# Performance work log

Hardware: AMD Instinct MI355X
Metric: run time of the kernel (lower is better)

Reference implementation:

```python
import jax, jax.numpy as jnp
import numpy as np

N_NODES = 50000
N_EDGES = 800000
D_IN = 128
HIDDEN = 64
N_CLASSES = 2


def gcn_conv(x, edge_index, W, b, num_nodes):
    """PyG GCNConv: linear (no bias) -> add self-loops -> sym-normalized aggregate -> + bias."""
    h = x @ W  # [N, H]
    loop = jnp.arange(num_nodes, dtype=edge_index.dtype)
    src = jnp.concatenate([edge_index[0], loop])  # [E+N]
    dst = jnp.concatenate([edge_index[1], loop])
    deg = jax.ops.segment_sum(jnp.ones_like(dst, dtype=h.dtype), dst, num_segments=num_nodes)
    dinv = jnp.where(deg > 0, jax.lax.rsqrt(deg), 0.0)
    norm = dinv[src] * dinv[dst]  # [E+N]
    msg = h[src] * norm[:, None]  # [E+N, H]  (gather + scale)
    out = jax.ops.segment_sum(msg, dst, num_segments=num_nodes)  # scatter-add
    return out + b


def setup_inputs() -> dict:
    key = jax.random.key(0)
    ks = jax.random.split(key, 6)
    x = jax.random.normal(ks[0], (N_NODES, D_IN), dtype=jnp.float32)
    edge_index = jax.random.randint(ks[1], (2, N_EDGES), 0, N_NODES, dtype=jnp.int64)
    # Glorot-ish init for weights, zero bias (PyG default)
    W1 = jax.random.normal(ks[2], (D_IN, HIDDEN), dtype=jnp.float32) * (1.0 / np.sqrt(D_IN))
    b1 = jnp.zeros((HIDDEN,), dtype=jnp.float32)
    W2 = jax.random.normal(ks[3], (HIDDEN, N_CLASSES), dtype=jnp.float32) * (1.0 / np.sqrt(HIDDEN))
    b2 = jnp.zeros((N_CLASSES,), dtype=jnp.float32)
    return {"x": x, "edge_index": edge_index, "W1": W1, "b1": b1, "W2": W2, "b2": b2}


def reference(x, edge_index, W1, b1, W2, b2):
    h = jax.nn.relu(gcn_conv(x, edge_index, W1, b1, N_NODES))
    # F.dropout(training=self.training) is identity in eval mode
    out = gcn_conv(h, edge_index, W2, b2, N_NODES)
    return out
```

## Files before the change

### kernel.cpp

```cpp
#include <hip/hip_runtime.h>

#define N_NODES 50000
#define N_EDGES 800000
#define D_IN 128
#define HIDDEN 64
#define N_CLASSES 2
#define NBUK 782
#define NBUK_P 784
#define NBLK 196
#define NBLK_P 200
#define NE4 200000
#define XPAD 136

typedef _Float16 half4v __attribute__((ext_vector_type(4)));
typedef _Float16 h8 __attribute__((ext_vector_type(8)));
typedef float f4 __attribute__((ext_vector_type(4)));


__global__ __launch_bounds__(256) void k_hist(const int4* __restrict__ dst4,
                                              int* __restrict__ bhist) {
    __shared__ int hist[NBUK];
    int t = threadIdx.x;
    for (int i = t; i < NBUK; i += 256) hist[i] = 0;
    __syncthreads();
    int base4 = blockIdx.x * 1024;
#pragma unroll
    for (int k = 0; k < 4; k++) {
        int idx = base4 + k * 256 + t;
        if (idx < NE4) {
            int4 d = dst4[idx];
            atomicAdd(&hist[d.x >> 6], 1);
            atomicAdd(&hist[d.y >> 6], 1);
            atomicAdd(&hist[d.z >> 6], 1);
            atomicAdd(&hist[d.w >> 6], 1);
        }
    }
    __syncthreads();
    for (int i = t; i < NBUK; i += 256) bhist[blockIdx.x * NBUK_P + i] = hist[i];
}


__global__ __launch_bounds__(256) void k_colscan(const int* __restrict__ bhist,
                                                 int* __restrict__ excT,
                                                 int* __restrict__ colsum) {
    __shared__ int part[256];
    int b = blockIdx.x;
    int t = threadIdx.x;
    int v = (t < NBLK) ? bhist[t * NBUK_P + b] : 0;
    part[t] = v;
    __syncthreads();
    for (int off = 1; off < 256; off <<= 1) {
        int p = (t >= off) ? part[t - off] : 0;
        __syncthreads();
        part[t] += p;
        __syncthreads();
    }
    if (t < NBLK) excT[b * NBLK_P + t] = part[t] - v;
    if (t == 255) colsum[b] = part[255];
}


__global__ __launch_bounds__(256) void k_binA2s(const int4* __restrict__ src4,
                                                const int4* __restrict__ dst4,
                                                const int* __restrict__ excT,
                                                const int* __restrict__ colsum,
                                                int* __restrict__ bucket_off,
                                                int* __restrict__ row_ptr,
                                                int* __restrict__ ebin) {
    __shared__ int part[256];
    __shared__ int cur[NBUK];
    const int b = blockIdx.x;
    const int t = threadIdx.x;

    int v[4];
    int s = 0;
#pragma unroll
    for (int i = 0; i < 4; i++) {
        int idx = t * 4 + i;
        v[i] = (idx < NBUK) ? colsum[idx] : 0;
        s += v[i];
    }
    part[t] = s;
    __syncthreads();
    for (int off = 1; off < 256; off <<= 1) {
        int p = (t >= off) ? part[t - off] : 0;
        __syncthreads();
        part[t] += p;
        __syncthreads();
    }
    int run = (t == 0) ? 0 : part[t - 1];
#pragma unroll
    for (int i = 0; i < 4; i++) {
        int idx = t * 4 + i;
        if (idx < NBUK) {
            cur[idx] = run + excT[idx * NBLK_P + b];
            if (b == 0) bucket_off[idx] = run;
            run += v[i];
        } else if (idx == NBUK && b == 0) {
            bucket_off[idx] = run;
        }
    }
    if (b == 0 && t == 0) row_ptr[N_NODES] = N_EDGES;
    __syncthreads();

    int base4 = b * 1024;
#pragma unroll
    for (int k = 0; k < 4; k++) {
        int idx = base4 + k * 256 + t;
        if (idx < NE4) {
            int4 sv = src4[idx];
            int4 d = dst4[idx];
            int p0 = atomicAdd(&cur[d.x >> 6], 1);
            int p1 = atomicAdd(&cur[d.y >> 6], 1);
            int p2 = atomicAdd(&cur[d.z >> 6], 1);
            int p3 = atomicAdd(&cur[d.w >> 6], 1);
            ebin[p0] = (sv.x << 7) | (d.x & 63);
            ebin[p1] = (sv.y << 7) | (d.y & 63);
            ebin[p2] = (sv.z << 7) | (d.z & 63);
            ebin[p3] = (sv.w << 7) | (d.w & 63);
        }
    }
}


__global__ __launch_bounds__(256) void k_csr_gemm(
    const int* __restrict__ ebin, const int* __restrict__ bucket_off,
    const float* __restrict__ x, const float* __restrict__ W1,
    int* __restrict__ row_ptr, float* __restrict__ dinv_g,
    int* __restrict__ rec, _Float16* __restrict__ hs)
{
    __shared__ _Float16 xs[64 * XPAD];
    __shared__ _Float16 Wt[64 * XPAD];
    __shared__ int cnt[64];
    __shared__ int cur[64];
    __shared__ float sdinv[64];
    const int b = blockIdx.x;
    const int t = threadIdx.x;
    const int row0 = b * 64;

    for (int i4 = t; i4 < 64 * D_IN / 4; i4 += 256) {
        int r = i4 >> 5;
        int k4 = (i4 & 31) << 2;
        int grow = row0 + r;
        half4v hv;
        if (grow < N_NODES) {
            float4 v = *(const float4*)&x[grow * D_IN + k4];
            hv.x = (_Float16)v.x; hv.y = (_Float16)v.y;
            hv.z = (_Float16)v.z; hv.w = (_Float16)v.w;
        } else {
            hv.x = hv.y = hv.z = hv.w = (_Float16)0.f;
        }
        *(half4v*)&xs[r * XPAD + k4] = hv;
    }
    for (int i4 = t; i4 < D_IN * HIDDEN / 4; i4 += 256) {
        float4 v = *(const float4*)&W1[i4 * 4];
        int k = i4 >> 4;
        int n = (i4 & 15) << 2;
        Wt[(n + 0) * XPAD + k] = (_Float16)v.x;
        Wt[(n + 1) * XPAD + k] = (_Float16)v.y;
        Wt[(n + 2) * XPAD + k] = (_Float16)v.z;
        Wt[(n + 3) * XPAD + k] = (_Float16)v.w;
    }

    if (t < 64) cnt[t] = 0;
    __syncthreads();
    int beg = bucket_off[b], end = bucket_off[b + 1];
    for (int i = beg + t; i < end; i += 256) atomicAdd(&cnt[ebin[i] & 63], 1);
    __syncthreads();
    if (t < 64) {
        int deg = cnt[t];
        int sum = deg;
#pragma unroll
        for (int off = 1; off < 64; off <<= 1) {
            int v = __shfl_up(sum, off, 64);
            if (t >= off) sum += v;
        }
        int rp = beg + sum - deg;
        cur[t] = rp;
        float di = rsqrtf((float)(deg + 1));
        sdinv[t] = di;
        int node = row0 + t;
        if (node < N_NODES) {
            row_ptr[node] = rp;
            dinv_g[node] = di;
        }
    }
    __syncthreads();
    for (int i = beg + t; i < end; i += 256) {
        int pk = ebin[i];
        int pos = atomicAdd(&cur[pk & 63], 1);
        rec[pos] = pk >> 7;
    }
    __syncthreads();

    const int w = t >> 6;
    const int L = t & 63;
    const int mrow = w * 16 + (L & 15);
    const int qk = (L >> 4) * 8;
    f4 acc0 = {0.f, 0.f, 0.f, 0.f}, acc1 = acc0, acc2 = acc0, acc3 = acc0;
#pragma unroll
    for (int ks = 0; ks < D_IN; ks += 32) {
        h8 a = *(const h8*)&xs[mrow * XPAD + ks + qk];
        h8 b0 = *(const h8*)&Wt[(0 * 16 + (L & 15)) * XPAD + ks + qk];
        h8 b1 = *(const h8*)&Wt[(1 * 16 + (L & 15)) * XPAD + ks + qk];
        h8 b2 = *(const h8*)&Wt[(2 * 16 + (L & 15)) * XPAD + ks + qk];
        h8 b3 = *(const h8*)&Wt[(3 * 16 + (L & 15)) * XPAD + ks + qk];
        acc0 = __builtin_amdgcn_mfma_f32_16x16x32_f16(a, b0, acc0, 0, 0, 0);
        acc1 = __builtin_amdgcn_mfma_f32_16x16x32_f16(a, b1, acc1, 0, 0, 0);
        acc2 = __builtin_amdgcn_mfma_f32_16x16x32_f16(a, b2, acc2, 0, 0, 0);
        acc3 = __builtin_amdgcn_mfma_f32_16x16x32_f16(a, b3, acc3, 0, 0, 0);
    }

    const int n0 = L & 15;
#pragma unroll
    for (int j = 0; j < 4; j++) {
        int m = w * 16 + (L >> 4) * 4 + j;
        float di = sdinv[m];
        size_t base = (size_t)(row0 + m) * HIDDEN;
        hs[base + 0 * 16 + n0] = (_Float16)(acc0[j] * di);
        hs[base + 1 * 16 + n0] = (_Float16)(acc1[j] * di);
        hs[base + 2 * 16 + n0] = (_Float16)(acc2[j] * di);
        hs[base + 3 * 16 + n0] = (_Float16)(acc3[j] * di);
    }
}


__global__ __launch_bounds__(256) void k_agg1_l2(
    const _Float16* __restrict__ hs, const int* __restrict__ row_ptr,
    const int* __restrict__ rec, const float* __restrict__ dinv,
    const float* __restrict__ b1, const float* __restrict__ W2,
    float* __restrict__ zs)
{
    const int node = blockIdx.x * 16 + (threadIdx.x >> 4);
    const int g = threadIdx.x & 15;
    const int gbase = threadIdx.x & 48;
    const half4v* H = (const half4v*)hs;

    float di = dinv[node];
    float4 acc = make_float4(0.f, 0.f, 0.f, 0.f);

    int beg = row_ptr[node];
    int end = row_ptr[node + 1];

    for (int base = beg; base < end; base += 16) {
        int n = end - base;
        if (n > 16) n = 16;
        int r = N_NODES;
        if (g < n) r = rec[base + g];
        int n8 = (n + 7) & ~7;
        for (int e = 0; e < n8; e += 8) {
            int i0 = gbase + e;
            int s0 = __shfl(r, i0 + 0, 64);
            int s1 = __shfl(r, i0 + 1, 64);
            int s2 = __shfl(r, i0 + 2, 64);
            int s3 = __shfl(r, i0 + 3, 64);
            int s4 = __shfl(r, i0 + 4, 64);
            int s5 = __shfl(r, i0 + 5, 64);
            int s6 = __shfl(r, i0 + 6, 64);
            int s7 = __shfl(r, i0 + 7, 64);
            half4v a0 = H[s0 * 16 + g];
            half4v a1 = H[s1 * 16 + g];
            half4v a2 = H[s2 * 16 + g];
            half4v a3 = H[s3 * 16 + g];
            half4v a4 = H[s4 * 16 + g];
            half4v a5 = H[s5 * 16 + g];
            half4v a6 = H[s6 * 16 + g];
            half4v a7 = H[s7 * 16 + g];
            acc.x += ((float)a0.x + (float)a1.x) + ((float)a2.x + (float)a3.x)
                   + ((float)a4.x + (float)a5.x) + ((float)a6.x + (float)a7.x);
            acc.y += ((float)a0.y + (float)a1.y) + ((float)a2.y + (float)a3.y)
                   + ((float)a4.y + (float)a5.y) + ((float)a6.y + (float)a7.y);
            acc.z += ((float)a0.z + (float)a1.z) + ((float)a2.z + (float)a3.z)
                   + ((float)a4.z + (float)a5.z) + ((float)a6.z + (float)a7.z);
            acc.w += ((float)a0.w + (float)a1.w) + ((float)a2.w + (float)a3.w)
                   + ((float)a4.w + (float)a5.w) + ((float)a6.w + (float)a7.w);
        }
    }

    half4v sv = H[node * 16 + g];
    acc.x += (float)sv.x;
    acc.y += (float)sv.y;
    acc.z += (float)sv.z;
    acc.w += (float)sv.w;

    float4 bb = ((const float4*)b1)[g];
    float4 y;
    y.x = fmaxf(fmaf(acc.x, di, bb.x), 0.f);
    y.y = fmaxf(fmaf(acc.y, di, bb.y), 0.f);
    y.z = fmaxf(fmaf(acc.z, di, bb.z), 0.f);
    y.w = fmaxf(fmaf(acc.w, di, bb.w), 0.f);
    float4 wA = ((const float4*)W2)[2 * g];
    float4 wB = ((const float4*)W2)[2 * g + 1];
    float p0 = y.x * wA.x + y.y * wA.z + y.z * wB.x + y.w * wB.z;
    float p1 = y.x * wA.y + y.y * wA.w + y.z * wB.y + y.w * wB.w;

    p0 += __shfl_down(p0, 8, 64);
    p1 += __shfl_down(p1, 8, 64);
    p0 += __shfl_down(p0, 4, 64);
    p1 += __shfl_down(p1, 4, 64);
    p0 += __shfl_down(p0, 2, 64);
    p1 += __shfl_down(p1, 2, 64);
    p0 += __shfl_down(p0, 1, 64);
    p1 += __shfl_down(p1, 1, 64);
    if (g == 0) {
        zs[node * 2 + 0] = p0 * di;
        zs[node * 2 + 1] = p1 * di;
    }
}


__global__ __launch_bounds__(256) void k_agg2(
    const float* __restrict__ zs, const int* __restrict__ row_ptr,
    const int* __restrict__ rec, const float* __restrict__ dinv,
    const float* __restrict__ b2, float* __restrict__ out)
{
    const int node = blockIdx.x * 32 + (threadIdx.x >> 3);
    const int j = threadIdx.x & 7;
    if (node >= N_NODES) return;
    int beg = row_ptr[node];
    int end = row_ptr[node + 1];
    float a0 = 0.f, a1 = 0.f;
    for (int idx = beg + j; idx < end; idx += 8) {
        int s = rec[idx];
        float2 v = *(const float2*)&zs[s * 2];
        a0 += v.x;
        a1 += v.y;
    }
    a0 += __shfl_down(a0, 4, 64);
    a1 += __shfl_down(a1, 4, 64);
    a0 += __shfl_down(a0, 2, 64);
    a1 += __shfl_down(a1, 2, 64);
    a0 += __shfl_down(a0, 1, 64);
    a1 += __shfl_down(a1, 1, 64);
    if (j == 0) {
        float di = dinv[node];
        float2 zv = *(const float2*)&zs[node * 2];
        float2 o;
        o.x = fmaf(di, a0 + zv.x, b2[0]);
        o.y = fmaf(di, a1 + zv.y, b2[1]);
        *(float2*)&out[node * 2] = o;
    }
}


extern "C" void kernel_launch(void* const* d_in, const int* in_sizes, int n_in,
                              void* d_out, int out_size, void* d_ws, size_t ws_size,
                              hipStream_t stream) {
    const float* x  = (const float*)d_in[0];
    const int* ei   = (const int*)d_in[1];
    const float* W1 = (const float*)d_in[2];
    const float* b1 = (const float*)d_in[3];
    const float* W2 = (const float*)d_in[4];
    const float* b2 = (const float*)d_in[5];
    float* out = (float*)d_out;

    const int4* src4 = (const int4*)ei;
    const int4* dst4 = (const int4*)(ei + N_EDGES);

    int*      bucket_off = (int*)d_ws;
    int*      colsum     = (int*)d_ws + 1024;
    float*    dinv       = (float*)d_ws + 2048;
    int*      row_ptr    = (int*)d_ws + 52224;
    int*      bhist      = (int*)d_ws + 102432;
    int*      excT       = (int*)d_ws + 256128;
    int*      ebin       = (int*)d_ws + 412576;
    int*      rec        = (int*)d_ws + 1212576;
    _Float16* hs         = (_Float16*)((int*)d_ws + 2012576);
    float*    zs         = (float*)d_ws + 3614112;

    k_hist<<<NBLK, 256, 0, stream>>>(dst4, bhist);
    k_colscan<<<NBUK, 256, 0, stream>>>(bhist, excT, colsum);
    k_binA2s<<<NBLK, 256, 0, stream>>>(src4, dst4, excT, colsum, bucket_off, row_ptr, ebin);
    k_csr_gemm<<<NBUK, 256, 0, stream>>>(ebin, bucket_off, x, W1, row_ptr, dinv, rec, hs);
    k_agg1_l2<<<N_NODES / 16, 256, 0, stream>>>(hs, row_ptr, rec, dinv, b1, W2, zs);
    k_agg2<<<(N_NODES + 31) / 32, 256, 0, stream>>>(zs, row_ptr, rec, dinv, b2, out);
}
```

Measured before the change: 129.7 us.

## Merge histogram with GEMM launch and fold column scan into binning kernel

The dense x@W1 GEMM now runs in the same launch as the edge-bucket histogram, as extra blocks, so it no longer waits behind the CSR build. The separate column-scan kernel is gone: each binning block recomputes its prefix and total from the per-block histograms by looping over all 196 rows. The degree scaling moves into a pass that re-reads and rewrites hs after the CSR build. This drops one launch and lets independent work overlap, at the cost of redundant histogram reads in every binning block and an extra read-modify-write of hs.

```diff
diff --git a/kernel.cpp b/kernel.cpp
--- a/kernel.cpp
+++ b/kernel.cpp
@@ -8,7 +8,6 @@
 #define NBUK 782
 #define NBUK_P 784
 #define NBLK 196
-#define NBLK_P 200
 #define NE4 200000
 #define XPAD 136
 
@@ -17,37 +16,123 @@
 typedef float f4 __attribute__((ext_vector_type(4)));
 
 
-__global__ __launch_bounds__(256) void k_hist(const int4* __restrict__ dst4,
-                                              int* __restrict__ bhist) {
-    __shared__ int hist[NBUK];
-    int t = threadIdx.x;
-    for (int i = t; i < NBUK; i += 256) hist[i] = 0;
-    __syncthreads();
-    int base4 = blockIdx.x * 1024;
-#pragma unroll
-    for (int k = 0; k < 4; k++) {
-        int idx = base4 + k * 256 + t;
-        if (idx < NE4) {
-            int4 d = dst4[idx];
-            atomicAdd(&hist[d.x >> 6], 1);
-            atomicAdd(&hist[d.y >> 6], 1);
-            atomicAdd(&hist[d.z >> 6], 1);
-            atomicAdd(&hist[d.w >> 6], 1);
-        }
-    }
-    __syncthreads();
-    for (int i = t; i < NBUK; i += 256) bhist[blockIdx.x * NBUK_P + i] = hist[i];
-}
-
-
-__global__ __launch_bounds__(256) void k_colscan(const int* __restrict__ bhist,
-                                                 int* __restrict__ excT,
-                                                 int* __restrict__ colsum) {
+__global__ __launch_bounds__(256) void k_hist_gemm(
+    const int4* __restrict__ dst4, int* __restrict__ bhist,
+    const float* __restrict__ x, const float* __restrict__ W1,
+    _Float16* __restrict__ hs)
+{
+    __shared__ __attribute__((aligned(16))) _Float16 smem[2 * 64 * XPAD];
+    const int t = threadIdx.x;
+
+    if (blockIdx.x < NBLK) {
+        int* hist = (int*)smem;
+        for (int i = t; i < NBUK_P; i += 256) hist[i] = 0;
+        __syncthreads();
+        int base4 = blockIdx.x * 1024;
+#pragma unroll
+        for (int k = 0; k < 4; k++) {
+            int idx = base4 + k * 256 + t;
+            if (idx < NE4) {
+                int4 d = dst4[idx];
+                atomicAdd(&hist[d.x >> 6], 1);
+                atomicAdd(&hist[d.y >> 6], 1);
+                atomicAdd(&hist[d.z >> 6], 1);
+                atomicAdd(&hist[d.w >> 6], 1);
+            }
+        }
+        __syncthreads();
+        for (int i = t; i < NBUK_P; i += 256) bhist[blockIdx.x * NBUK_P + i] = hist[i];
+        return;
+    }
+
+    _Float16* xs = smem;
+    _Float16* Wt = smem + 64 * XPAD;
+    const int gb = blockIdx.x - NBLK;
+    const int row0 = gb * 64;
+
+    for (int i4 = t; i4 < 64 * D_IN / 4; i4 += 256) {
+        int r = i4 >> 5;
+        int k4 = (i4 & 31) << 2;
+        int grow = row0 + r;
+        half4v hv;
+        if (grow < N_NODES) {
+            float4 v = *(const float4*)&x[grow * D_IN + k4];
+            hv.x = (_Float16)v.x; hv.y = (_Float16)v.y;
+            hv.z = (_Float16)v.z; hv.w = (_Float16)v.w;
+        } else {
+            hv.x = hv.y = hv.z = hv.w = (_Float16)0.f;
+        }
+        *(half4v*)&xs[r * XPAD + k4] = hv;
+    }
+    for (int i4 = t; i4 < D_IN * HIDDEN / 4; i4 += 256) {
+        float4 v = *(const float4*)&W1[i4 * 4];
+        int k = i4 >> 4;
+        int n = (i4 & 15) << 2;
+        Wt[(n + 0) * XPAD + k] = (_Float16)v.x;
+        Wt[(n + 1) * XPAD + k] = (_Float16)v.y;
+        Wt[(n + 2) * XPAD + k] = (_Float16)v.z;
+        Wt[(n + 3) * XPAD + k] = (_Float16)v.w;
+    }
+    __syncthreads();
+
+    const int w = t >> 6;
+    const int L = t & 63;
+    const int mrow = w * 16 + (L & 15);
+    const int qk = (L >> 4) * 8;
+    f4 acc0 = {0.f, 0.f, 0.f, 0.f}, acc1 = acc0, acc2 = acc0, acc3 = acc0;
+#pragma unroll
+    for (int ks = 0; ks < D_IN; ks += 32) {
+        h8 a  = *(const h8*)&xs[mrow * XPAD + ks + qk];
+        h8 b0 = *(const h8*)&Wt[(0 * 16 + (L & 15)) * XPAD + ks + qk];
+        h8 b1 = *(const h8*)&Wt[(1 * 16 + (L & 15)) * XPAD + ks + qk];
+        h8 b2 = *(const h8*)&Wt[(2 * 16 + (L & 15)) * XPAD + ks + qk];
+        h8 b3 = *(const h8*)&Wt[(3 * 16 + (L & 15)) * XPAD + ks + qk];
+        acc0 = __builtin_amdgcn_mfma_f32_16x16x32_f16(a, b0, acc0, 0, 0, 0);
+        acc1 = __builtin_amdgcn_mfma_f32_16x16x32_f16(a, b1, acc1, 0, 0, 0);
+        acc2 = __builtin_amdgcn_mfma_f32_16x16x32_f16(a, b2, acc2, 0, 0, 0);
+        acc3 = __builtin_amdgcn_mfma_f32_16x16x32_f16(a, b3, acc3, 0, 0, 0);
+    }
+
+    const int n0 = L & 15;
+#pragma unroll
+    for (int j = 0; j < 4; j++) {
+        int m = w * 16 + (L >> 4) * 4 + j;
+        size_t base = (size_t)(row0 + m) * HIDDEN;
+        hs[base + 0 * 16 + n0] = (_Float16)acc0[j];
+        hs[base + 1 * 16 + n0] = (_Float16)acc1[j];
+        hs[base + 2 * 16 + n0] = (_Float16)acc2[j];
+        hs[base + 3 * 16 + n0] = (_Float16)acc3[j];
+    }
+}
+
+
+__global__ __launch_bounds__(256) void k_scan_bin(
+    const int4* __restrict__ src4, const int4* __restrict__ dst4,
+    const int* __restrict__ bhist,
+    int* __restrict__ bucket_off, int* __restrict__ row_ptr,
+    int* __restrict__ ebin)
+{
     __shared__ int part[256];
-    int b = blockIdx.x;
-    int t = threadIdx.x;
-    int v = (t < NBLK) ? bhist[t * NBUK_P + b] : 0;
-    part[t] = v;
+    __shared__ int cur[NBUK];
+    const int b = blockIdx.x;
+    const int t = threadIdx.x;
+
+    int4 pre = {0, 0, 0, 0};
+    int4 tot = {0, 0, 0, 0};
+    if (t < NBUK_P / 4) {
+        const int4* bh4 = (const int4*)bhist;
+        for (int c = 0; c < b; c++) {
+            int4 h = bh4[c * (NBUK_P / 4) + t];
+            pre.x += h.x; pre.y += h.y; pre.z += h.z; pre.w += h.w;
+        }
+        tot = pre;
+        for (int c = b; c < NBLK; c++) {
+            int4 h = bh4[c * (NBUK_P / 4) + t];
+            tot.x += h.x; tot.y += h.y; tot.z += h.z; tot.w += h.w;
+        }
+    }
+    int s = tot.x + tot.y + tot.z + tot.w;
+    part[t] = s;
     __syncthreads();
     for (int off = 1; off < 256; off <<= 1) {
         int p = (t >= off) ? part[t - off] : 0;
@@ -55,49 +140,16 @@
         part[t] += p;
         __syncthreads();
     }
-    if (t < NBLK) excT[b * NBLK_P + t] = part[t] - v;
-    if (t == 255) colsum[b] = part[255];
-}
-
-
-__global__ __launch_bounds__(256) void k_binA2s(const int4* __restrict__ src4,
-                                                const int4* __restrict__ dst4,
-                                                const int* __restrict__ excT,
-                                                const int* __restrict__ colsum,
-                                                int* __restrict__ bucket_off,
-                                                int* __restrict__ row_ptr,
-                                                int* __restrict__ ebin) {
-    __shared__ int part[256];
-    __shared__ int cur[NBUK];
-    const int b = blockIdx.x;
-    const int t = threadIdx.x;
-
-    int v[4];
-    int s = 0;
+    int run = (t == 0) ? 0 : part[t - 1];
+    int v[4]  = {tot.x, tot.y, tot.z, tot.w};
+    int pr[4] = {pre.x, pre.y, pre.z, pre.w};
 #pragma unroll
     for (int i = 0; i < 4; i++) {
         int idx = t * 4 + i;
-        v[i] = (idx < NBUK) ? colsum[idx] : 0;
-        s += v[i];
-    }
-    part[t] = s;
-    __syncthreads();
-    for (int off = 1; off < 256; off <<= 1) {
-        int p = (t >= off) ? part[t - off] : 0;
-        __syncthreads();
-        part[t] += p;
-        __syncthreads();
-    }
-    int run = (t == 0) ? 0 : part[t - 1];
-#pragma unroll
-    for (int i = 0; i < 4; i++) {
-        int idx = t * 4 + i;
-        if (idx < NBUK) {
-            cur[idx] = run + excT[idx * NBLK_P + b];
-            if (b == 0) bucket_off[idx] = run;
+        if (idx < NBUK_P) {
+            if (idx < NBUK) cur[idx] = run + pr[i];
+            if (b == 0 && idx <= NBUK) bucket_off[idx] = run;
             run += v[i];
-        } else if (idx == NBUK && b == 0) {
-            bucket_off[idx] = run;
         }
     }
     if (b == 0 && t == 0) row_ptr[N_NODES] = N_EDGES;
@@ -123,44 +175,17 @@
 }
 
 
-__global__ __launch_bounds__(256) void k_csr_gemm(
+__global__ __launch_bounds__(256) void k_csr_scale(
     const int* __restrict__ ebin, const int* __restrict__ bucket_off,
-    const float* __restrict__ x, const float* __restrict__ W1,
     int* __restrict__ row_ptr, float* __restrict__ dinv_g,
     int* __restrict__ rec, _Float16* __restrict__ hs)
 {
-    __shared__ _Float16 xs[64 * XPAD];
-    __shared__ _Float16 Wt[64 * XPAD];
     __shared__ int cnt[64];
     __shared__ int cur[64];
     __shared__ float sdinv[64];
     const int b = blockIdx.x;
     const int t = threadIdx.x;
     const int row0 = b * 64;
-
-    for (int i4 = t; i4 < 64 * D_IN / 4; i4 += 256) {
-        int r = i4 >> 5;
-        int k4 = (i4 & 31) << 2;
-        int grow = row0 + r;
-        half4v hv;
-        if (grow < N_NODES) {
-            float4 v = *(const float4*)&x[grow * D_IN + k4];
-            hv.x = (_Float16)v.x; hv.y = (_Float16)v.y;
-            hv.z = (_Float16)v.z; hv.w = (_Float16)v.w;
-        } else {
-            hv.x = hv.y = hv.z = hv.w = (_Float16)0.f;
-        }
-        *(half4v*)&xs[r * XPAD + k4] = hv;
-    }
-    for (int i4 = t; i4 < D_IN * HIDDEN / 4; i4 += 256) {
-        float4 v = *(const float4*)&W1[i4 * 4];
-        int k = i4 >> 4;
-        int n = (i4 & 15) << 2;
-        Wt[(n + 0) * XPAD + k] = (_Float16)v.x;
-        Wt[(n + 1) * XPAD + k] = (_Float16)v.y;
-        Wt[(n + 2) * XPAD + k] = (_Float16)v.z;
-        Wt[(n + 3) * XPAD + k] = (_Float16)v.w;
-    }
 
     if (t < 64) cnt[t] = 0;
     __syncthreads();
@@ -191,36 +216,15 @@
         int pos = atomicAdd(&cur[pk & 63], 1);
         rec[pos] = pk >> 7;
     }
-    __syncthreads();
-
-    const int w = t >> 6;
-    const int L = t & 63;
-    const int mrow = w * 16 + (L & 15);
-    const int qk = (L >> 4) * 8;
-    f4 acc0 = {0.f, 0.f, 0.f, 0.f}, acc1 = acc0, acc2 = acc0, acc3 = acc0;
-#pragma unroll
-    for (int ks = 0; ks < D_IN; ks += 32) {
-        h8 a = *(const h8*)&xs[mrow * XPAD + ks + qk];
-        h8 b0 = *(const h8*)&Wt[(0 * 16 + (L & 15)) * XPAD + ks + qk];
-        h8 b1 = *(const h8*)&Wt[(1 * 16 + (L & 15)) * XPAD + ks + qk];
-        h8 b2 = *(const h8*)&Wt[(2 * 16 + (L & 15)) * XPAD + ks + qk];
-        h8 b3 = *(const h8*)&Wt[(3 * 16 + (L & 15)) * XPAD + ks + qk];
-        acc0 = __builtin_amdgcn_mfma_f32_16x16x32_f16(a, b0, acc0, 0, 0, 0);
-        acc1 = __builtin_amdgcn_mfma_f32_16x16x32_f16(a, b1, acc1, 0, 0, 0);
-        acc2 = __builtin_amdgcn_mfma_f32_16x16x32_f16(a, b2, acc2, 0, 0, 0);
-        acc3 = __builtin_amdgcn_mfma_f32_16x16x32_f16(a, b3, acc3, 0, 0, 0);
-    }
-
-    const int n0 = L & 15;
-#pragma unroll
-    for (int j = 0; j < 4; j++) {
-        int m = w * 16 + (L >> 4) * 4 + j;
-        float di = sdinv[m];
-        size_t base = (size_t)(row0 + m) * HIDDEN;
-        hs[base + 0 * 16 + n0] = (_Float16)(acc0[j] * di);
-        hs[base + 1 * 16 + n0] = (_Float16)(acc1[j] * di);
-        hs[base + 2 * 16 + n0] = (_Float16)(acc2[j] * di);
-        hs[base + 3 * 16 + n0] = (_Float16)(acc3[j] * di);
+    for (int i = t; i < 64 * HIDDEN / 8; i += 256) {
+        int r = i >> 3;
+        int c = (i & 7) << 3;
+        size_t base = (size_t)(row0 + r) * HIDDEN + c;
+        h8 hv = *(const h8*)&hs[base];
+        float di = sdinv[r];
+#pragma unroll
+        for (int k = 0; k < 8; k++) hv[k] = (_Float16)((float)hv[k] * di);
+        *(h8*)&hs[base] = hv;
     }
 }
 
@@ -358,20 +362,17 @@
     const int4* dst4 = (const int4*)(ei + N_EDGES);
 
     int*      bucket_off = (int*)d_ws;
-    int*      colsum     = (int*)d_ws + 1024;
     float*    dinv       = (float*)d_ws + 2048;
     int*      row_ptr    = (int*)d_ws + 52224;
     int*      bhist      = (int*)d_ws + 102432;
-    int*      excT       = (int*)d_ws + 256128;
     int*      ebin       = (int*)d_ws + 412576;
     int*      rec        = (int*)d_ws + 1212576;
     _Float16* hs         = (_Float16*)((int*)d_ws + 2012576);
     float*    zs         = (float*)d_ws + 3614112;
 
-    k_hist<<<NBLK, 256, 0, stream>>>(dst4, bhist);
-    k_colscan<<<NBUK, 256, 0, stream>>>(bhist, excT, colsum);
-    k_binA2s<<<NBLK, 256, 0, stream>>>(src4, dst4, excT, colsum, bucket_off, row_ptr, ebin);
-    k_csr_gemm<<<NBUK, 256, 0, stream>>>(ebin, bucket_off, x, W1, row_ptr, dinv, rec, hs);
+    k_hist_gemm<<<NBLK + NBUK, 256, 0, stream>>>(dst4, bhist, x, W1, hs);
+    k_scan_bin<<<NBLK, 256, 0, stream>>>(src4, dst4, bhist, bucket_off, row_ptr, ebin);
+    k_csr_scale<<<NBUK, 256, 0, stream>>>(ebin, bucket_off, row_ptr, dinv, rec, hs);
     k_agg1_l2<<<N_NODES / 16, 256, 0, stream>>>(hs, row_ptr, rec, dinv, b1, W2, zs);
     k_agg2<<<(N_NODES + 31) / 32, 256, 0, stream>>>(zs, row_ptr, rec, dinv, b2, out);
 }
```

After: 155.7 us. 20.1% more time.

## Move layer-1 GEMM into histogram kernel, apply degree scaling in CSR pass

Applied to the files above, without the earlier changes.

The dense x·W1 MFMA GEMM now runs as extra blocks of the histogram launch, so it executes alongside the edge histogram instead of after binning. The CSR-building kernel no longer stages x and W1. It rereads the fp16 GEMM output and rescales each row in place by the inverse-sqrt degree. This takes GEMM work off the critical path of the dependent kernel chain, at the cost of an extra read-modify-write of hs and a second fp16 rounding of each value.

```diff
diff --git a/kernel.cpp b/kernel.cpp
--- a/kernel.cpp
+++ b/kernel.cpp
@@ -17,26 +17,93 @@
 typedef float f4 __attribute__((ext_vector_type(4)));
 
 
-__global__ __launch_bounds__(256) void k_hist(const int4* __restrict__ dst4,
-                                              int* __restrict__ bhist) {
-    __shared__ int hist[NBUK];
-    int t = threadIdx.x;
-    for (int i = t; i < NBUK; i += 256) hist[i] = 0;
-    __syncthreads();
-    int base4 = blockIdx.x * 1024;
-#pragma unroll
-    for (int k = 0; k < 4; k++) {
-        int idx = base4 + k * 256 + t;
-        if (idx < NE4) {
-            int4 d = dst4[idx];
-            atomicAdd(&hist[d.x >> 6], 1);
-            atomicAdd(&hist[d.y >> 6], 1);
-            atomicAdd(&hist[d.z >> 6], 1);
-            atomicAdd(&hist[d.w >> 6], 1);
-        }
-    }
-    __syncthreads();
-    for (int i = t; i < NBUK; i += 256) bhist[blockIdx.x * NBUK_P + i] = hist[i];
+__global__ __launch_bounds__(256) void k_hist_gemm(
+    const int4* __restrict__ dst4, int* __restrict__ bhist,
+    const float* __restrict__ x, const float* __restrict__ W1,
+    _Float16* __restrict__ hs)
+{
+    __shared__ __attribute__((aligned(16))) _Float16 smem[2 * 64 * XPAD];
+    const int t = threadIdx.x;
+
+    if (blockIdx.x < NBLK) {
+        int* hist = (int*)smem;
+        for (int i = t; i < NBUK_P; i += 256) hist[i] = 0;
+        __syncthreads();
+        int base4 = blockIdx.x * 1024;
+#pragma unroll
+        for (int k = 0; k < 4; k++) {
+            int idx = base4 + k * 256 + t;
+            if (idx < NE4) {
+                int4 d = dst4[idx];
+                atomicAdd(&hist[d.x >> 6], 1);
+                atomicAdd(&hist[d.y >> 6], 1);
+                atomicAdd(&hist[d.z >> 6], 1);
+                atomicAdd(&hist[d.w >> 6], 1);
+            }
+        }
+        __syncthreads();
+        for (int i = t; i < NBUK_P; i += 256) bhist[blockIdx.x * NBUK_P + i] = hist[i];
+        return;
+    }
+
+    _Float16* xs = smem;
+    _Float16* Wt = smem + 64 * XPAD;
+    const int gb = blockIdx.x - NBLK;
+    const int row0 = gb * 64;
+
+    for (int i4 = t; i4 < 64 * D_IN / 4; i4 += 256) {
+        int r = i4 >> 5;
+        int k4 = (i4 & 31) << 2;
+        int grow = row0 + r;
+        half4v hv;
+        if (grow < N_NODES) {
+            float4 v = *(const float4*)&x[grow * D_IN + k4];
+            hv.x = (_Float16)v.x; hv.y = (_Float16)v.y;
+            hv.z = (_Float16)v.z; hv.w = (_Float16)v.w;
+        } else {
+            hv.x = hv.y = hv.z = hv.w = (_Float16)0.f;
+        }
+        *(half4v*)&xs[r * XPAD + k4] = hv;
+    }
+    for (int i4 = t; i4 < D_IN * HIDDEN / 4; i4 += 256) {
+        float4 v = *(const float4*)&W1[i4 * 4];
+        int k = i4 >> 4;
+        int n = (i4 & 15) << 2;
+        Wt[(n + 0) * XPAD + k] = (_Float16)v.x;
+        Wt[(n + 1) * XPAD + k] = (_Float16)v.y;
+        Wt[(n + 2) * XPAD + k] = (_Float16)v.z;
+        Wt[(n + 3) * XPAD + k] = (_Float16)v.w;
+    }
+    __syncthreads();
+
+    const int w = t >> 6;
+    const int L = t & 63;
+    const int mrow = w * 16 + (L & 15);
+    const int qk = (L >> 4) * 8;
+    f4 acc0 = {0.f, 0.f, 0.f, 0.f}, acc1 = acc0, acc2 = acc0, acc3 = acc0;
+#pragma unroll
+    for (int ks = 0; ks < D_IN; ks += 32) {
+        h8 a  = *(const h8*)&xs[mrow * XPAD + ks + qk];
+        h8 b0 = *(const h8*)&Wt[(0 * 16 + (L & 15)) * XPAD + ks + qk];
+        h8 b1 = *(const h8*)&Wt[(1 * 16 + (L & 15)) * XPAD + ks + qk];
+        h8 b2 = *(const h8*)&Wt[(2 * 16 + (L & 15)) * XPAD + ks + qk];
+        h8 b3 = *(const h8*)&Wt[(3 * 16 + (L & 15)) * XPAD + ks + qk];
+        acc0 = __builtin_amdgcn_mfma_f32_16x16x32_f16(a, b0, acc0, 0, 0, 0);
+        acc1 = __builtin_amdgcn_mfma_f32_16x16x32_f16(a, b1, acc1, 0, 0, 0);
+        acc2 = __builtin_amdgcn_mfma_f32_16x16x32_f16(a, b2, acc2, 0, 0, 0);
+        acc3 = __builtin_amdgcn_mfma_f32_16x16x32_f16(a, b3, acc3, 0, 0, 0);
+    }
+
+    const int n0 = L & 15;
+#pragma unroll
+    for (int j = 0; j < 4; j++) {
+        int m = w * 16 + (L >> 4) * 4 + j;
+        size_t base = (size_t)(row0 + m) * HIDDEN;
+        hs[base + 0 * 16 + n0] = (_Float16)acc0[j];
+        hs[base + 1 * 16 + n0] = (_Float16)acc1[j];
+        hs[base + 2 * 16 + n0] = (_Float16)acc2[j];
+        hs[base + 3 * 16 + n0] = (_Float16)acc3[j];
+    }
 }
 
 
@@ -123,44 +190,17 @@
 }
 
 
-__global__ __launch_bounds__(256) void k_csr_gemm(
+__global__ __launch_bounds__(256) void k_csr_scale(
     const int* __restrict__ ebin, const int* __restrict__ bucket_off,
-    const float* __restrict__ x, const float* __restrict__ W1,
     int* __restrict__ row_ptr, float* __restrict__ dinv_g,
     int* __restrict__ rec, _Float16* __restrict__ hs)
 {
-    __shared__ _Float16 xs[64 * XPAD];
-    __shared__ _Float16 Wt[64 * XPAD];
     __shared__ int cnt[64];
     __shared__ int cur[64];
     __shared__ float sdinv[64];
     const int b = blockIdx.x;
     const int t = threadIdx.x;
     const int row0 = b * 64;
-
-    for (int i4 = t; i4 < 64 * D_IN / 4; i4 += 256) {
-        int r = i4 >> 5;
-        int k4 = (i4 & 31) << 2;
-        int grow = row0 + r;
-        half4v hv;
-        if (grow < N_NODES) {
-            float4 v = *(const float4*)&x[grow * D_IN + k4];
-            hv.x = (_Float16)v.x; hv.y = (_Float16)v.y;
-            hv.z = (_Float16)v.z; hv.w = (_Float16)v.w;
-        } else {
-            hv.x = hv.y = hv.z = hv.w = (_Float16)0.f;
-        }
-        *(half4v*)&xs[r * XPAD + k4] = hv;
-    }
-    for (int i4 = t; i4 < D_IN * HIDDEN / 4; i4 += 256) {
-        float4 v = *(const float4*)&W1[i4 * 4];
-        int k = i4 >> 4;
-        int n = (i4 & 15) << 2;
-        Wt[(n + 0) * XPAD + k] = (_Float16)v.x;
-        Wt[(n + 1) * XPAD + k] = (_Float16)v.y;
-        Wt[(n + 2) * XPAD + k] = (_Float16)v.z;
-        Wt[(n + 3) * XPAD + k] = (_Float16)v.w;
-    }
 
     if (t < 64) cnt[t] = 0;
     __syncthreads();
@@ -191,36 +231,15 @@
         int pos = atomicAdd(&cur[pk & 63], 1);
         rec[pos] = pk >> 7;
     }
-    __syncthreads();
-
-    const int w = t >> 6;
-    const int L = t & 63;
-    const int mrow = w * 16 + (L & 15);
-    const int qk = (L >> 4) * 8;
-    f4 acc0 = {0.f, 0.f, 0.f, 0.f}, acc1 = acc0, acc2 = acc0, acc3 = acc0;
-#pragma unroll
-    for (int ks = 0; ks < D_IN; ks += 32) {
-        h8 a = *(const h8*)&xs[mrow * XPAD + ks + qk];
-        h8 b0 = *(const h8*)&Wt[(0 * 16 + (L & 15)) * XPAD + ks + qk];
-        h8 b1 = *(const h8*)&Wt[(1 * 16 + (L & 15)) * XPAD + ks + qk];
-        h8 b2 = *(const h8*)&Wt[(2 * 16 + (L & 15)) * XPAD + ks + qk];
-        h8 b3 = *(const h8*)&Wt[(3 * 16 + (L & 15)) * XPAD + ks + qk];
-        acc0 = __builtin_amdgcn_mfma_f32_16x16x32_f16(a, b0, acc0, 0, 0, 0);
-        acc1 = __builtin_amdgcn_mfma_f32_16x16x32_f16(a, b1, acc1, 0, 0, 0);
-        acc2 = __builtin_amdgcn_mfma_f32_16x16x32_f16(a, b2, acc2, 0, 0, 0);
-        acc3 = __builtin_amdgcn_mfma_f32_16x16x32_f16(a, b3, acc3, 0, 0, 0);
-    }
-
-    const int n0 = L & 15;
-#pragma unroll
-    for (int j = 0; j < 4; j++) {
-        int m = w * 16 + (L >> 4) * 4 + j;
-        float di = sdinv[m];
-        size_t base = (size_t)(row0 + m) * HIDDEN;
-        hs[base + 0 * 16 + n0] = (_Float16)(acc0[j] * di);
-        hs[base + 1 * 16 + n0] = (_Float16)(acc1[j] * di);
-        hs[base + 2 * 16 + n0] = (_Float16)(acc2[j] * di);
-        hs[base + 3 * 16 + n0] = (_Float16)(acc3[j] * di);
+    for (int i = t; i < 64 * HIDDEN / 8; i += 256) {
+        int r = i >> 3;
+        int c = (i & 7) << 3;
+        size_t base = (size_t)(row0 + r) * HIDDEN + c;
+        h8 hv = *(const h8*)&hs[base];
+        float di = sdinv[r];
+#pragma unroll
+        for (int k = 0; k < 8; k++) hv[k] = (_Float16)((float)hv[k] * di);
+        *(h8*)&hs[base] = hv;
     }
 }
 
@@ -368,10 +387,10 @@
     _Float16* hs         = (_Float16*)((int*)d_ws + 2012576);
     float*    zs         = (float*)d_ws + 3614112;
 
-    k_hist<<<NBLK, 256, 0, stream>>>(dst4, bhist);
+    k_hist_gemm<<<NBLK + NBUK, 256, 0, stream>>>(dst4, bhist, x, W1, hs);
     k_colscan<<<NBUK, 256, 0, stream>>>(bhist, excT, colsum);
     k_binA2s<<<NBLK, 256, 0, stream>>>(src4, dst4, excT, colsum, bucket_off, row_ptr, ebin);
-    k_csr_gemm<<<NBUK, 256, 0, stream>>>(ebin, bucket_off, x, W1, row_ptr, dinv, rec, hs);
+    k_csr_scale<<<NBUK, 256, 0, stream>>>(ebin, bucket_off, row_ptr, dinv, rec, hs);
     k_agg1_l2<<<N_NODES / 16, 256, 0, stream>>>(hs, row_ptr, rec, dinv, b1, W2, zs);
     k_agg2<<<(N_NODES + 31) / 32, 256, 0, stream>>>(zs, row_ptr, rec, dinv, b2, out);
 }
```

Result: no change. 128.9 us (-0.6%).
